# Kernel tuning notes

Measured on AMD Instinct MI355X. Metric: run time of the kernel, lower is better.

## Reference

```python
import jax, jax.numpy as jnp
import numpy as np

HIDDEN = 1024
HEADS = 16
HEAD_D = HIDDEN // HEADS
FILL = -10000.0


def setup_inputs() -> dict:
    key = jax.random.key(0)
    ks = jax.random.split(key, 5)
    scale = 1.0 / np.sqrt(HIDDEN)
    x = jax.random.normal(ks[0], (2, 2048, HIDDEN), dtype=jnp.float32)
    # nn.Linear weights stored as [in, out] (already transposed vs torch)
    W_qkv = jax.random.uniform(ks[1], (HIDDEN, 3 * HIDDEN), dtype=jnp.float32, minval=-scale, maxval=scale)
    b_qkv = jax.random.uniform(ks[2], (3 * HIDDEN,), dtype=jnp.float32, minval=-scale, maxval=scale)
    W_o = jax.random.uniform(ks[3], (HIDDEN, HIDDEN), dtype=jnp.float32, minval=-scale, maxval=scale)
    b_o = jax.random.uniform(ks[4], (HIDDEN,), dtype=jnp.float32, minval=-scale, maxval=scale)
    return {"x": x, "W_qkv": W_qkv, "b_qkv": b_qkv, "W_o": W_o, "b_o": b_o}


def reference(x, W_qkv, b_qkv, W_o, b_o):
    b, s, _ = x.shape
    qkv = x @ W_qkv + b_qkv                       # [b, s, 3*hidden]
    q, k, v = jnp.split(qkv, 3, axis=-1)
    # [b, s, hidden] -> [b, h, s, d]
    def to_heads(t):
        return t.reshape(b, s, HEADS, HEAD_D).transpose(0, 2, 1, 3)
    q, k, v = to_heads(q), to_heads(k), to_heads(v)
    logits = jnp.einsum('bhqd,bhkd->bhqk', q, k) / np.sqrt(HEAD_D).astype(np.float32)
    # Faithful to the original: tril, then fill anything equal to 0 (incl.
    # genuine zeros) with the masked_logit_fill value.
    logits_tril = jnp.tril(logits)
    logits_masked = jnp.where(logits_tril == 0.0, jnp.float32(FILL), logits_tril)
    probs = jax.nn.softmax(logits_masked, axis=-1)
    pre_o = jnp.einsum('bhqk,bhkd->bhqd', probs, v)    # [b, h, s, d]
    pre_o = pre_o.transpose(0, 2, 1, 3).reshape(b, s, HIDDEN)
    return pre_o @ W_o + b_o
```

## Files before the change

### kernel.cpp

```cpp
#include <hip/hip_runtime.h>

typedef __attribute__((ext_vector_type(8))) short short8;
typedef __attribute__((ext_vector_type(4))) short short4b;
typedef __attribute__((ext_vector_type(4))) float f32x4;

static __device__ __forceinline__ short f2bf(float f) {
    unsigned u = __builtin_bit_cast(unsigned, f);
    u += 0x7FFFu + ((u >> 16) & 1u);
    return (short)(u >> 16);
}

static __device__ __forceinline__ void g2l16(const void* g, void* l) {
    __builtin_amdgcn_global_load_lds(
        (const __attribute__((address_space(1))) unsigned*)g,
        (__attribute__((address_space(3))) unsigned*)l, 16, 0, 0);
}

__global__ void convert_x(const float* __restrict__ x, short* __restrict__ xb, int n4) {
    int i = blockIdx.x * blockDim.x + threadIdx.x;
    if (i >= n4) return;
    f32x4 v = *(const f32x4*)&x[(long)i * 4];
    short4b o;
    #pragma unroll
    for (int j = 0; j < 4; ++j) o[j] = f2bf(v[j]);
    *(short4b*)&xb[(long)i * 4] = o;
}

__global__ void transpose_conv(const float* __restrict__ W, short* __restrict__ Wt,
                               int K, int N) {
    __shared__ float lds[64][65];
    const int t = threadIdx.x;
    const int n0 = blockIdx.x * 64, k0 = blockIdx.y * 64;
    const int rr = t >> 4, q4 = (t & 15) * 4;
    #pragma unroll
    for (int p = 0; p < 4; ++p) {
        int k = rr + p * 16;
        f32x4 v = *(const f32x4*)&W[(long)(k0 + k) * N + n0 + q4];
        #pragma unroll
        for (int j = 0; j < 4; ++j) lds[k][q4 + j] = v[j];
    }
    __syncthreads();
    #pragma unroll
    for (int p = 0; p < 4; ++p) {
        int nloc = rr + p * 16;
        short4b o;
        #pragma unroll
        for (int j = 0; j < 4; ++j) o[j] = f2bf(lds[q4 + j][nloc]);
        *(short4b*)&Wt[(long)(n0 + nloc) * K + k0 + q4] = o;
    }
}

template<int F32OUT>
__global__ __launch_bounds__(256, 2)
void gemm_bt(const short* __restrict__ A, const short* __restrict__ Bt,
             const float* __restrict__ bias, void* __restrict__ C,
             int M, int N, int K) {
    __shared__ short lA[128 * 32];
    __shared__ short lB[128 * 32];
    const int t = threadIdx.x;
    const int lane = t & 63, w = t >> 6;
    const int m0 = blockIdx.y * 128, n0 = blockIdx.x * 128;
    const int lr = lane & 15, lk = lane >> 4;
    const int wr = w >> 1, wc = w & 1;

    f32x4 acc[4][4];
    #pragma unroll
    for (int i = 0; i < 4; ++i)
        #pragma unroll
        for (int j = 0; j < 4; ++j)
            #pragma unroll
            for (int e = 0; e < 4; ++e) acc[i][j][e] = 0.0f;

    const int nsteps = K >> 5;
    for (int kt = 0; kt < nsteps; ++kt) {
        const int kb = kt * 32;
        #pragma unroll
        for (int c = 0; c < 2; ++c) {
            int off  = c * 4096 + w * 1024;
            int offl = off + lane * 16;
            int ra = offl >> 6;
            int ca = (offl & 63) >> 1;
            g2l16(A  + (long)(m0 + ra) * K + kb + ca, (short*)lA + (off >> 1));
            g2l16(Bt + (long)(n0 + ra) * K + kb + ca, (short*)lB + (off >> 1));
        }
        __syncthreads();
        short8 af[4], bf[4];
        #pragma unroll
        for (int m = 0; m < 4; ++m)
            af[m] = *(const short8*)&lA[(wr * 64 + m * 16 + lr) * 32 + lk * 8];
        #pragma unroll
        for (int n = 0; n < 4; ++n)
            bf[n] = *(const short8*)&lB[(wc * 64 + n * 16 + lr) * 32 + lk * 8];
        #pragma unroll
        for (int m = 0; m < 4; ++m)
            #pragma unroll
            for (int n = 0; n < 4; ++n)
                acc[m][n] = __builtin_amdgcn_mfma_f32_16x16x32_bf16(af[m], bf[n], acc[m][n], 0, 0, 0);
        __syncthreads();
    }

    #pragma unroll
    for (int n = 0; n < 4; ++n) {
        int col = n0 + wc * 64 + n * 16 + lr;
        float bb = bias[col];
        #pragma unroll
        for (int m = 0; m < 4; ++m) {
            int rowb = m0 + wr * 64 + m * 16 + lk * 4;
            #pragma unroll
            for (int r = 0; r < 4; ++r) {
                float v = acc[m][n][r] + bb;
                if (F32OUT) ((float*)C)[(long)(rowb + r) * N + col] = v;
                else        ((short*)C)[(long)(rowb + r) * N + col] = f2bf(v);
            }
        }
    }
}

__global__ void build_vt(const short* __restrict__ qkv, short* __restrict__ vt) {
    __shared__ short lds[64][72];
    const int t = threadIdx.x;
    const int st = blockIdx.x, bh = blockIdx.y;
    const int b = bh >> 4, h = bh & 15;
    const int s0 = st * 64;
    const int sr = t >> 3, c8 = (t & 7) * 8;
    #pragma unroll
    for (int p = 0; p < 2; ++p) {
        int s = sr + p * 32;
        short8 v = *(const short8*)&qkv[(long)(b * 2048 + s0 + s) * 3072 + 2048 + h * 64 + c8];
        *(short8*)&lds[s][c8] = v;
    }
    __syncthreads();
    #pragma unroll
    for (int p = 0; p < 2; ++p) {
        int d = sr + p * 32;
        short8 v;
        #pragma unroll
        for (int j = 0; j < 8; ++j) v[j] = lds[c8 + j][d];
        *(short8*)&vt[(long)(bh * 64 + d) * 2048 + s0 + c8] = v;
    }
}

__global__ __launch_bounds__(256, 2)
void attn_kernel(const short* __restrict__ qkv, const short* __restrict__ vt,
                 short* __restrict__ pre_o) {
    __shared__ short lK[2][64 * 64];
    __shared__ short lV[2][64 * 64];
    __shared__ short lP[4][16 * 64];
    const int t = threadIdx.x, lane = t & 63, w = t >> 6;
    const int lr = lane & 15, lk = lane >> 4;
    const int pidx = blockIdx.x, bh = blockIdx.y;
    const int b = bh >> 4, h = bh & 15;

    int soff[2], sK_row[2], sslot[2];
    #pragma unroll
    for (int c = 0; c < 2; ++c) {
        int off  = c * 4096 + w * 1024;
        int offl = off + lane * 16;
        int r    = offl >> 7;
        soff[c]  = off >> 1;
        sK_row[c] = r;
        sslot[c] = (((offl >> 4) & 7) ^ (r & 7)) * 8;
    }

    #pragma unroll 1
    for (int seg = 0; seg < 2; ++seg) {
        const int Q  = seg ? (31 - pidx) : pidx;
        const int q0 = Q * 64;
        const int nt = seg ? (32 - pidx) : (pidx + 1);

        short8 aq[2];
        #pragma unroll
        for (int dk = 0; dk < 2; ++dk)
            aq[dk] = *(const short8*)&qkv[(long)(b * 2048 + q0 + w * 16 + lr) * 3072
                                          + h * 64 + dk * 32 + lk * 8];

        f32x4 accO[4];
        #pragma unroll
        for (int n = 0; n < 4; ++n)
            #pragma unroll
            for (int e = 0; e < 4; ++e) accO[n][e] = 0.0f;
        float mst[4], lst[4];
        #pragma unroll
        for (int r = 0; r < 4; ++r) { mst[r] = -1e30f; lst[r] = 0.0f; }

        #pragma unroll
        for (int c = 0; c < 2; ++c) {
            g2l16(qkv + (long)(b * 2048 + 0 * 64 + sK_row[c]) * 3072 + 1024 + h * 64 + sslot[c],
                  &lK[0][soff[c]]);
            g2l16(vt + (long)(bh * 64 + sK_row[c]) * 2048 + 0 * 64 + sslot[c],
                  &lV[0][soff[c]]);
        }
        __syncthreads();

        #pragma unroll 1
        for (int kt = 0; kt < nt; ++kt) {
            const int cur = kt & 1;
            if (kt + 1 < nt) {
                #pragma unroll
                for (int c = 0; c < 2; ++c) {
                    g2l16(qkv + (long)(b * 2048 + (kt + 1) * 64 + sK_row[c]) * 3072
                              + 1024 + h * 64 + sslot[c],
                          &lK[cur ^ 1][soff[c]]);
                    g2l16(vt + (long)(bh * 64 + sK_row[c]) * 2048 + (kt + 1) * 64 + sslot[c],
                          &lV[cur ^ 1][soff[c]]);
                }
            }

            f32x4 accS[4];
            #pragma unroll
            for (int n = 0; n < 4; ++n)
                #pragma unroll
                for (int e = 0; e < 4; ++e) accS[n][e] = 0.0f;
            short8 bk[4][2];
            #pragma unroll
            for (int n = 0; n < 4; ++n)
                #pragma unroll
                for (int dk = 0; dk < 2; ++dk)
                    bk[n][dk] = *(const short8*)((const char*)&lK[cur][0] + (n * 16 + lr) * 128
                                                 + (((dk * 4 + lk) ^ (lr & 7)) << 4));
            #pragma unroll
            for (int n = 0; n < 4; ++n)
                #pragma unroll
                for (int dk = 0; dk < 2; ++dk)
                    accS[n] = __builtin_amdgcn_mfma_f32_16x16x32_bf16(aq[dk], bk[n][dk], accS[n], 0, 0, 0);

            #pragma unroll
            for (int r = 0; r < 4; ++r) {
                int qrow = q0 + w * 16 + lk * 4 + r;
                float sv[4];
                float mx = -1e30f;
                #pragma unroll
                for (int n = 0; n < 4; ++n) {
                    float s = accS[n][r] * 0.125f;
                    int key = kt * 64 + n * 16 + lr;
                    if (key > qrow || s == 0.0f) s = -10000.0f;
                    sv[n] = s;
                    mx = fmaxf(mx, s);
                }
                mx = fmaxf(mx, __shfl_xor(mx, 1));
                mx = fmaxf(mx, __shfl_xor(mx, 2));
                mx = fmaxf(mx, __shfl_xor(mx, 4));
                mx = fmaxf(mx, __shfl_xor(mx, 8));
                float mnew = fmaxf(mst[r], mx);
                float corr = __expf(mst[r] - mnew);
                mst[r] = mnew;
                float rs = 0.0f;
                #pragma unroll
                for (int n = 0; n < 4; ++n) { float p = __expf(sv[n] - mnew); sv[n] = p; rs += p; }
                rs += __shfl_xor(rs, 1);
                rs += __shfl_xor(rs, 2);
                rs += __shfl_xor(rs, 4);
                rs += __shfl_xor(rs, 8);
                lst[r] = lst[r] * corr + rs;
                #pragma unroll
                for (int n = 0; n < 4; ++n) accO[n][r] *= corr;
                int prr = lk * 4 + r;
                int swz = (prr & 7) << 4;
                #pragma unroll
                for (int n = 0; n < 4; ++n) {
                    int pc = n * 16 + lr;
                    *(short*)((char*)&lP[w][0] + prr * 128 + ((pc * 2) ^ swz)) = f2bf(sv[n]);
                }
            }

            short8 ap[2], bv[4][2];
            #pragma unroll
            for (int kk = 0; kk < 2; ++kk)
                ap[kk] = *(const short8*)((const char*)&lP[w][0] + lr * 128
                                          + (((kk * 4 + lk) ^ (lr & 7)) << 4));
            #pragma unroll
            for (int n = 0; n < 4; ++n)
                #pragma unroll
                for (int kk = 0; kk < 2; ++kk)
                    bv[n][kk] = *(const short8*)((const char*)&lV[cur][0] + (n * 16 + lr) * 128
                                                 + (((kk * 4 + lk) ^ (lr & 7)) << 4));
            #pragma unroll
            for (int n = 0; n < 4; ++n)
                #pragma unroll
                for (int kk = 0; kk < 2; ++kk)
                    accO[n] = __builtin_amdgcn_mfma_f32_16x16x32_bf16(ap[kk], bv[n][kk], accO[n], 0, 0, 0);

            __syncthreads();
        }

        #pragma unroll
        for (int r = 0; r < 4; ++r) {
            int qrow = q0 + w * 16 + lk * 4 + r;
            float inv = 1.0f / lst[r];
            #pragma unroll
            for (int n = 0; n < 4; ++n)
                pre_o[(long)(b * 2048 + qrow) * 1024 + h * 64 + n * 16 + lr] =
                    f2bf(accO[n][r] * inv);
        }
    }
}

extern "C" void kernel_launch(void* const* d_in, const int* in_sizes, int n_in,
                              void* d_out, int out_size, void* d_ws, size_t ws_size,
                              hipStream_t stream) {
    const float* x    = (const float*)d_in[0];
    const float* Wqkv = (const float*)d_in[1];
    const float* bqkv = (const float*)d_in[2];
    const float* Wo   = (const float*)d_in[3];
    const float* bo   = (const float*)d_in[4];
    float* out = (float*)d_out;

    char* ws = (char*)d_ws;
    short* xb    = (short*)(ws);
    short* wqkvT = (short*)(ws + (8L  << 20));
    short* woT   = (short*)(ws + (14L << 20));
    short* qkv   = (short*)(ws + (16L << 20));
    short* vt    = (short*)(ws + (40L << 20));
    short* preo  = (short*)(ws + (48L << 20));

    convert_x<<<4096, 256, 0, stream>>>(x, xb, 4096 * 1024 / 4);
    transpose_conv<<<dim3(48, 16), 256, 0, stream>>>(Wqkv, wqkvT, 1024, 3072);
    transpose_conv<<<dim3(16, 16), 256, 0, stream>>>(Wo, woT, 1024, 1024);
    gemm_bt<0><<<dim3(24, 32), 256, 0, stream>>>(xb, wqkvT, bqkv, qkv, 4096, 3072, 1024);
    build_vt<<<dim3(32, 32), 256, 0, stream>>>(qkv, vt);
    attn_kernel<<<dim3(16, 32), 256, 0, stream>>>(qkv, vt, preo);
    gemm_bt<1><<<dim3(8, 32), 256, 0, stream>>>(preo, woT, bo, out, 4096, 1024, 1024);
}
```

Baseline: 224.6 us.

## Use 128-key tiles in attention, fold Q scaling into QKV GEMM, mask only diagonal

The attention inner loop now processes 128 keys per iteration instead of 64, which halves the number of barriers and online-softmax rescale steps and doubles the K/V tiles staged in LDS with wider swizzles. The 1/sqrt(d) scale is moved into the QKV GEMM epilogue for the Q columns, so the attention loop no longer multiplies by it. Causal masking is evaluated only on the final diagonal tile. In exchange, LDS usage and register pressure go up, which may reduce occupancy. The diagonal tile now also computes some fully masked keys. Because Q is rounded to bf16 after scaling by 0.125, the zero-equality fill check could behave slightly differently.

```diff
diff --git a/kernel.cpp b/kernel.cpp
--- a/kernel.cpp
+++ b/kernel.cpp
@@ -50,7 +50,7 @@
     }
 }
 
-template<int F32OUT>
+template<int F32OUT, int QSCALE>
 __global__ __launch_bounds__(256, 2)
 void gemm_bt(const short* __restrict__ A, const short* __restrict__ Bt,
              const float* __restrict__ bias, void* __restrict__ C,
@@ -103,12 +103,13 @@
     for (int n = 0; n < 4; ++n) {
         int col = n0 + wc * 64 + n * 16 + lr;
         float bb = bias[col];
+        float sc = (QSCALE && col < 1024) ? 0.125f : 1.0f;
         #pragma unroll
         for (int m = 0; m < 4; ++m) {
             int rowb = m0 + wr * 64 + m * 16 + lk * 4;
             #pragma unroll
             for (int r = 0; r < 4; ++r) {
-                float v = acc[m][n][r] + bb;
+                float v = (acc[m][n][r] + bb) * sc;
                 if (F32OUT) ((float*)C)[(long)(rowb + r) * N + col] = v;
                 else        ((short*)C)[(long)(rowb + r) * N + col] = f2bf(v);
             }
@@ -143,30 +144,33 @@
 __global__ __launch_bounds__(256, 2)
 void attn_kernel(const short* __restrict__ qkv, const short* __restrict__ vt,
                  short* __restrict__ pre_o) {
-    __shared__ short lK[2][64 * 64];
-    __shared__ short lV[2][64 * 64];
-    __shared__ short lP[4][16 * 64];
+    __shared__ short lK[2][128 * 64];
+    __shared__ short lV[2][64 * 128];
+    __shared__ short lP[4][16 * 128];
     const int t = threadIdx.x, lane = t & 63, w = t >> 6;
     const int lr = lane & 15, lk = lane >> 4;
     const int pidx = blockIdx.x, bh = blockIdx.y;
     const int b = bh >> 4, h = bh & 15;
 
-    int soff[2], sK_row[2], sslot[2];
-    #pragma unroll
-    for (int c = 0; c < 2; ++c) {
+    int soff[4], kRow[4], kCol[4], vRow[4], vCol[4];
+    #pragma unroll
+    for (int c = 0; c < 4; ++c) {
         int off  = c * 4096 + w * 1024;
         int offl = off + lane * 16;
-        int r    = offl >> 7;
-        soff[c]  = off >> 1;
-        sK_row[c] = r;
-        sslot[c] = (((offl >> 4) & 7) ^ (r & 7)) * 8;
+        soff[c] = off >> 1;
+        int kr = offl >> 7;
+        kRow[c] = kr;
+        kCol[c] = ((((offl >> 4) & 7) ^ (kr & 7))) * 8;
+        int vr = offl >> 8;
+        vRow[c] = vr;
+        vCol[c] = ((((offl >> 4) & 15) ^ (vr & 15))) * 8;
     }
 
     #pragma unroll 1
     for (int seg = 0; seg < 2; ++seg) {
         const int Q  = seg ? (31 - pidx) : pidx;
         const int q0 = Q * 64;
-        const int nt = seg ? (32 - pidx) : (pidx + 1);
+        const int nt = (Q >> 1) + 1;
 
         short8 aq[2];
         #pragma unroll
@@ -184,10 +188,10 @@
         for (int r = 0; r < 4; ++r) { mst[r] = -1e30f; lst[r] = 0.0f; }
 
         #pragma unroll
-        for (int c = 0; c < 2; ++c) {
-            g2l16(qkv + (long)(b * 2048 + 0 * 64 + sK_row[c]) * 3072 + 1024 + h * 64 + sslot[c],
+        for (int c = 0; c < 4; ++c) {
+            g2l16(qkv + (long)(b * 2048 + kRow[c]) * 3072 + 1024 + h * 64 + kCol[c],
                   &lK[0][soff[c]]);
-            g2l16(vt + (long)(bh * 64 + sK_row[c]) * 2048 + 0 * 64 + sslot[c],
+            g2l16(vt + (long)(bh * 64 + vRow[c]) * 2048 + vCol[c],
                   &lV[0][soff[c]]);
         }
         __syncthreads();
@@ -197,46 +201,47 @@
             const int cur = kt & 1;
             if (kt + 1 < nt) {
                 #pragma unroll
-                for (int c = 0; c < 2; ++c) {
-                    g2l16(qkv + (long)(b * 2048 + (kt + 1) * 64 + sK_row[c]) * 3072
-                              + 1024 + h * 64 + sslot[c],
+                for (int c = 0; c < 4; ++c) {
+                    g2l16(qkv + (long)(b * 2048 + (kt + 1) * 128 + kRow[c]) * 3072
+                              + 1024 + h * 64 + kCol[c],
                           &lK[cur ^ 1][soff[c]]);
-                    g2l16(vt + (long)(bh * 64 + sK_row[c]) * 2048 + (kt + 1) * 64 + sslot[c],
+                    g2l16(vt + (long)(bh * 64 + vRow[c]) * 2048 + (kt + 1) * 128 + vCol[c],
                           &lV[cur ^ 1][soff[c]]);
                 }
             }
 
-            f32x4 accS[4];
-            #pragma unroll
-            for (int n = 0; n < 4; ++n)
+            f32x4 accS[8];
+            #pragma unroll
+            for (int n = 0; n < 8; ++n) {
                 #pragma unroll
                 for (int e = 0; e < 4; ++e) accS[n][e] = 0.0f;
-            short8 bk[4][2];
-            #pragma unroll
-            for (int n = 0; n < 4; ++n)
-                #pragma unroll
-                for (int dk = 0; dk < 2; ++dk)
-                    bk[n][dk] = *(const short8*)((const char*)&lK[cur][0] + (n * 16 + lr) * 128
-                                                 + (((dk * 4 + lk) ^ (lr & 7)) << 4));
-            #pragma unroll
-            for (int n = 0; n < 4; ++n)
-                #pragma unroll
-                for (int dk = 0; dk < 2; ++dk)
-                    accS[n] = __builtin_amdgcn_mfma_f32_16x16x32_bf16(aq[dk], bk[n][dk], accS[n], 0, 0, 0);
-
+                #pragma unroll
+                for (int dk = 0; dk < 2; ++dk) {
+                    short8 bk = *(const short8*)((const char*)&lK[cur][0]
+                                 + (n * 16 + lr) * 128 + (((dk * 4 + lk) ^ (lr & 7)) << 4));
+                    accS[n] = __builtin_amdgcn_mfma_f32_16x16x32_bf16(aq[dk], bk, accS[n], 0, 0, 0);
+                }
+            }
+
+            const bool diag = (kt == nt - 1);
             #pragma unroll
             for (int r = 0; r < 4; ++r) {
                 int qrow = q0 + w * 16 + lk * 4 + r;
-                float sv[4];
-                float mx = -1e30f;
-                #pragma unroll
-                for (int n = 0; n < 4; ++n) {
-                    float s = accS[n][r] * 0.125f;
-                    int key = kt * 64 + n * 16 + lr;
-                    if (key > qrow || s == 0.0f) s = -10000.0f;
+                float sv[8];
+                #pragma unroll
+                for (int n = 0; n < 8; ++n) {
+                    float s = accS[n][r];
+                    if (diag) {
+                        int key = kt * 128 + n * 16 + lr;
+                        if (key > qrow || s == 0.0f) s = -10000.0f;
+                    } else {
+                        if (s == 0.0f) s = -10000.0f;
+                    }
                     sv[n] = s;
-                    mx = fmaxf(mx, s);
-                }
+                }
+                float mx01 = fmaxf(sv[0], sv[1]), mx23 = fmaxf(sv[2], sv[3]);
+                float mx45 = fmaxf(sv[4], sv[5]), mx67 = fmaxf(sv[6], sv[7]);
+                float mx = fmaxf(fmaxf(mx01, mx23), fmaxf(mx45, mx67));
                 mx = fmaxf(mx, __shfl_xor(mx, 1));
                 mx = fmaxf(mx, __shfl_xor(mx, 2));
                 mx = fmaxf(mx, __shfl_xor(mx, 4));
@@ -246,7 +251,7 @@
                 mst[r] = mnew;
                 float rs = 0.0f;
                 #pragma unroll
-                for (int n = 0; n < 4; ++n) { float p = __expf(sv[n] - mnew); sv[n] = p; rs += p; }
+                for (int n = 0; n < 8; ++n) { float p = __expf(sv[n] - mnew); sv[n] = p; rs += p; }
                 rs += __shfl_xor(rs, 1);
                 rs += __shfl_xor(rs, 2);
                 rs += __shfl_xor(rs, 4);
@@ -255,30 +260,27 @@
                 #pragma unroll
                 for (int n = 0; n < 4; ++n) accO[n][r] *= corr;
                 int prr = lk * 4 + r;
-                int swz = (prr & 7) << 4;
-                #pragma unroll
-                for (int n = 0; n < 4; ++n) {
+                int swz = (prr & 15) << 4;
+                #pragma unroll
+                for (int n = 0; n < 8; ++n) {
                     int pc = n * 16 + lr;
-                    *(short*)((char*)&lP[w][0] + prr * 128 + ((pc * 2) ^ swz)) = f2bf(sv[n]);
+                    *(short*)((char*)&lP[w][0] + prr * 256 + ((pc * 2) ^ swz)) = f2bf(sv[n]);
                 }
             }
 
-            short8 ap[2], bv[4][2];
-            #pragma unroll
-            for (int kk = 0; kk < 2; ++kk)
-                ap[kk] = *(const short8*)((const char*)&lP[w][0] + lr * 128
-                                          + (((kk * 4 + lk) ^ (lr & 7)) << 4));
+            short8 ap[4];
+            #pragma unroll
+            for (int kk = 0; kk < 4; ++kk)
+                ap[kk] = *(const short8*)((const char*)&lP[w][0] + lr * 256
+                                          + (((kk * 4 + lk) ^ (lr & 15)) << 4));
             #pragma unroll
             for (int n = 0; n < 4; ++n)
                 #pragma unroll
-                for (int kk = 0; kk < 2; ++kk)
-                    bv[n][kk] = *(const short8*)((const char*)&lV[cur][0] + (n * 16 + lr) * 128
-                                                 + (((kk * 4 + lk) ^ (lr & 7)) << 4));
-            #pragma unroll
-            for (int n = 0; n < 4; ++n)
-                #pragma unroll
-                for (int kk = 0; kk < 2; ++kk)
-                    accO[n] = __builtin_amdgcn_mfma_f32_16x16x32_bf16(ap[kk], bv[n][kk], accO[n], 0, 0, 0);
+                for (int kk = 0; kk < 4; ++kk) {
+                    short8 bv = *(const short8*)((const char*)&lV[cur][0]
+                                 + (n * 16 + lr) * 256 + (((kk * 4 + lk) ^ (lr & 15)) << 4));
+                    accO[n] = __builtin_amdgcn_mfma_f32_16x16x32_bf16(ap[kk], bv, accO[n], 0, 0, 0);
+                }
 
             __syncthreads();
         }
@@ -316,8 +318,8 @@
     convert_x<<<4096, 256, 0, stream>>>(x, xb, 4096 * 1024 / 4);
     transpose_conv<<<dim3(48, 16), 256, 0, stream>>>(Wqkv, wqkvT, 1024, 3072);
     transpose_conv<<<dim3(16, 16), 256, 0, stream>>>(Wo, woT, 1024, 1024);
-    gemm_bt<0><<<dim3(24, 32), 256, 0, stream>>>(xb, wqkvT, bqkv, qkv, 4096, 3072, 1024);
+    gemm_bt<0, 1><<<dim3(24, 32), 256, 0, stream>>>(xb, wqkvT, bqkv, qkv, 4096, 3072, 1024);
     build_vt<<<dim3(32, 32), 256, 0, stream>>>(qkv, vt);
     attn_kernel<<<dim3(16, 32), 256, 0, stream>>>(qkv, vt, preo);
-    gemm_bt<1><<<dim3(8, 32), 256, 0, stream>>>(preo, woT, bo, out, 4096, 1024, 1024);
-}
+    gemm_bt<1, 0><<<dim3(8, 32), 256, 0, stream>>>(preo, woT, bo, out, 4096, 1024, 1024);
+}
```

Result: no change. 229.0 us (+2.0%).

## Split attention into one block per query tile, fold scale into QKV GEMM

Applied to the files above, without the earlier changes.

The attention kernel no longer pairs a short and a long query tile in one block. It launches one block per 64-row query tile, with the heaviest tiles first, and raises launch bounds to four blocks per CU for more parallelism and occupancy. The 1/8 logit scale now happens in the QKV GEMM epilogue on the Q columns, and the causal index check runs only on the diagonal tile. Scaling Q before rounding to bf16 changes rounding slightly, and the exact-zero test now applies to the scaled product. Per-block prologue overhead doubles because there are twice as many blocks.

```diff
diff --git a/kernel.cpp b/kernel.cpp
--- a/kernel.cpp
+++ b/kernel.cpp
@@ -50,7 +50,7 @@
     }
 }
 
-template<int F32OUT>
+template<int F32OUT, int QSCALE>
 __global__ __launch_bounds__(256, 2)
 void gemm_bt(const short* __restrict__ A, const short* __restrict__ Bt,
              const float* __restrict__ bias, void* __restrict__ C,
@@ -103,12 +103,13 @@
     for (int n = 0; n < 4; ++n) {
         int col = n0 + wc * 64 + n * 16 + lr;
         float bb = bias[col];
+        float sc = (QSCALE && col < 1024) ? 0.125f : 1.0f;
         #pragma unroll
         for (int m = 0; m < 4; ++m) {
             int rowb = m0 + wr * 64 + m * 16 + lk * 4;
             #pragma unroll
             for (int r = 0; r < 4; ++r) {
-                float v = acc[m][n][r] + bb;
+                float v = (acc[m][n][r] + bb) * sc;
                 if (F32OUT) ((float*)C)[(long)(rowb + r) * N + col] = v;
                 else        ((short*)C)[(long)(rowb + r) * N + col] = f2bf(v);
             }
@@ -140,7 +141,7 @@
     }
 }
 
-__global__ __launch_bounds__(256, 2)
+__global__ __launch_bounds__(256, 4)
 void attn_kernel(const short* __restrict__ qkv, const short* __restrict__ vt,
                  short* __restrict__ pre_o) {
     __shared__ short lK[2][64 * 64];
@@ -148,150 +149,142 @@
     __shared__ short lP[4][16 * 64];
     const int t = threadIdx.x, lane = t & 63, w = t >> 6;
     const int lr = lane & 15, lk = lane >> 4;
-    const int pidx = blockIdx.x, bh = blockIdx.y;
+    const int Q = 31 - blockIdx.x;
+    const int bh = blockIdx.y;
     const int b = bh >> 4, h = bh & 15;
-
-    int soff[2], sK_row[2], sslot[2];
+    const int q0 = Q * 64;
+    const int nt = Q + 1;
+
+    int soff[2], sRow[2], sCol[2];
     #pragma unroll
     for (int c = 0; c < 2; ++c) {
         int off  = c * 4096 + w * 1024;
         int offl = off + lane * 16;
         int r    = offl >> 7;
         soff[c]  = off >> 1;
-        sK_row[c] = r;
-        sslot[c] = (((offl >> 4) & 7) ^ (r & 7)) * 8;
-    }
+        sRow[c]  = r;
+        sCol[c]  = (((offl >> 4) & 7) ^ (r & 7)) * 8;
+    }
+
+    short8 aq[2];
+    #pragma unroll
+    for (int dk = 0; dk < 2; ++dk)
+        aq[dk] = *(const short8*)&qkv[(long)(b * 2048 + q0 + w * 16 + lr) * 3072
+                                      + h * 64 + dk * 32 + lk * 8];
+
+    f32x4 accO[4];
+    #pragma unroll
+    for (int n = 0; n < 4; ++n)
+        #pragma unroll
+        for (int e = 0; e < 4; ++e) accO[n][e] = 0.0f;
+    float mst[4], lst[4];
+    #pragma unroll
+    for (int r = 0; r < 4; ++r) { mst[r] = -1e30f; lst[r] = 0.0f; }
+
+    #pragma unroll
+    for (int c = 0; c < 2; ++c) {
+        g2l16(qkv + (long)(b * 2048 + sRow[c]) * 3072 + 1024 + h * 64 + sCol[c],
+              &lK[0][soff[c]]);
+        g2l16(vt + (long)(bh * 64 + sRow[c]) * 2048 + sCol[c],
+              &lV[0][soff[c]]);
+    }
+    __syncthreads();
 
     #pragma unroll 1
-    for (int seg = 0; seg < 2; ++seg) {
-        const int Q  = seg ? (31 - pidx) : pidx;
-        const int q0 = Q * 64;
-        const int nt = seg ? (32 - pidx) : (pidx + 1);
-
-        short8 aq[2];
-        #pragma unroll
-        for (int dk = 0; dk < 2; ++dk)
-            aq[dk] = *(const short8*)&qkv[(long)(b * 2048 + q0 + w * 16 + lr) * 3072
-                                          + h * 64 + dk * 32 + lk * 8];
-
-        f32x4 accO[4];
-        #pragma unroll
-        for (int n = 0; n < 4; ++n)
-            #pragma unroll
-            for (int e = 0; e < 4; ++e) accO[n][e] = 0.0f;
-        float mst[4], lst[4];
-        #pragma unroll
-        for (int r = 0; r < 4; ++r) { mst[r] = -1e30f; lst[r] = 0.0f; }
-
-        #pragma unroll
-        for (int c = 0; c < 2; ++c) {
-            g2l16(qkv + (long)(b * 2048 + 0 * 64 + sK_row[c]) * 3072 + 1024 + h * 64 + sslot[c],
-                  &lK[0][soff[c]]);
-            g2l16(vt + (long)(bh * 64 + sK_row[c]) * 2048 + 0 * 64 + sslot[c],
-                  &lV[0][soff[c]]);
-        }
-        __syncthreads();
-
-        #pragma unroll 1
-        for (int kt = 0; kt < nt; ++kt) {
-            const int cur = kt & 1;
-            if (kt + 1 < nt) {
-                #pragma unroll
-                for (int c = 0; c < 2; ++c) {
-                    g2l16(qkv + (long)(b * 2048 + (kt + 1) * 64 + sK_row[c]) * 3072
-                              + 1024 + h * 64 + sslot[c],
-                          &lK[cur ^ 1][soff[c]]);
-                    g2l16(vt + (long)(bh * 64 + sK_row[c]) * 2048 + (kt + 1) * 64 + sslot[c],
-                          &lV[cur ^ 1][soff[c]]);
-                }
-            }
-
-            f32x4 accS[4];
-            #pragma unroll
-            for (int n = 0; n < 4; ++n)
-                #pragma unroll
-                for (int e = 0; e < 4; ++e) accS[n][e] = 0.0f;
-            short8 bk[4][2];
-            #pragma unroll
-            for (int n = 0; n < 4; ++n)
-                #pragma unroll
-                for (int dk = 0; dk < 2; ++dk)
-                    bk[n][dk] = *(const short8*)((const char*)&lK[cur][0] + (n * 16 + lr) * 128
-                                                 + (((dk * 4 + lk) ^ (lr & 7)) << 4));
-            #pragma unroll
-            for (int n = 0; n < 4; ++n)
-                #pragma unroll
-                for (int dk = 0; dk < 2; ++dk)
-                    accS[n] = __builtin_amdgcn_mfma_f32_16x16x32_bf16(aq[dk], bk[n][dk], accS[n], 0, 0, 0);
-
-            #pragma unroll
-            for (int r = 0; r < 4; ++r) {
-                int qrow = q0 + w * 16 + lk * 4 + r;
-                float sv[4];
-                float mx = -1e30f;
-                #pragma unroll
-                for (int n = 0; n < 4; ++n) {
-                    float s = accS[n][r] * 0.125f;
+    for (int kt = 0; kt < nt; ++kt) {
+        const int cur = kt & 1;
+        if (kt + 1 < nt) {
+            #pragma unroll
+            for (int c = 0; c < 2; ++c) {
+                g2l16(qkv + (long)(b * 2048 + (kt + 1) * 64 + sRow[c]) * 3072
+                          + 1024 + h * 64 + sCol[c],
+                      &lK[cur ^ 1][soff[c]]);
+                g2l16(vt + (long)(bh * 64 + sRow[c]) * 2048 + (kt + 1) * 64 + sCol[c],
+                      &lV[cur ^ 1][soff[c]]);
+            }
+        }
+
+        f32x4 accS[4];
+        #pragma unroll
+        for (int n = 0; n < 4; ++n) {
+            #pragma unroll
+            for (int e = 0; e < 4; ++e) accS[n][e] = 0.0f;
+            #pragma unroll
+            for (int dk = 0; dk < 2; ++dk) {
+                short8 bk = *(const short8*)((const char*)&lK[cur][0]
+                             + (n * 16 + lr) * 128 + (((dk * 4 + lk) ^ (lr & 7)) << 4));
+                accS[n] = __builtin_amdgcn_mfma_f32_16x16x32_bf16(aq[dk], bk, accS[n], 0, 0, 0);
+            }
+        }
+
+        const bool diag = (kt == nt - 1);
+        #pragma unroll
+        for (int r = 0; r < 4; ++r) {
+            int qrow = q0 + w * 16 + lk * 4 + r;
+            float sv[4];
+            #pragma unroll
+            for (int n = 0; n < 4; ++n) {
+                float s = accS[n][r];
+                if (diag) {
                     int key = kt * 64 + n * 16 + lr;
                     if (key > qrow || s == 0.0f) s = -10000.0f;
-                    sv[n] = s;
-                    mx = fmaxf(mx, s);
+                } else {
+                    if (s == 0.0f) s = -10000.0f;
                 }
-                mx = fmaxf(mx, __shfl_xor(mx, 1));
-                mx = fmaxf(mx, __shfl_xor(mx, 2));
-                mx = fmaxf(mx, __shfl_xor(mx, 4));
-                mx = fmaxf(mx, __shfl_xor(mx, 8));
-                float mnew = fmaxf(mst[r], mx);
-                float corr = __expf(mst[r] - mnew);
-                mst[r] = mnew;
-                float rs = 0.0f;
-                #pragma unroll
-                for (int n = 0; n < 4; ++n) { float p = __expf(sv[n] - mnew); sv[n] = p; rs += p; }
-                rs += __shfl_xor(rs, 1);
-                rs += __shfl_xor(rs, 2);
-                rs += __shfl_xor(rs, 4);
-                rs += __shfl_xor(rs, 8);
-                lst[r] = lst[r] * corr + rs;
-                #pragma unroll
-                for (int n = 0; n < 4; ++n) accO[n][r] *= corr;
-                int prr = lk * 4 + r;
-                int swz = (prr & 7) << 4;
-                #pragma unroll
-                for (int n = 0; n < 4; ++n) {
-                    int pc = n * 16 + lr;
-                    *(short*)((char*)&lP[w][0] + prr * 128 + ((pc * 2) ^ swz)) = f2bf(sv[n]);
-                }
-            }
-
-            short8 ap[2], bv[4][2];
-            #pragma unroll
-            for (int kk = 0; kk < 2; ++kk)
-                ap[kk] = *(const short8*)((const char*)&lP[w][0] + lr * 128
-                                          + (((kk * 4 + lk) ^ (lr & 7)) << 4));
-            #pragma unroll
-            for (int n = 0; n < 4; ++n)
-                #pragma unroll
-                for (int kk = 0; kk < 2; ++kk)
-                    bv[n][kk] = *(const short8*)((const char*)&lV[cur][0] + (n * 16 + lr) * 128
-                                                 + (((kk * 4 + lk) ^ (lr & 7)) << 4));
-            #pragma unroll
-            for (int n = 0; n < 4; ++n)
-                #pragma unroll
-                for (int kk = 0; kk < 2; ++kk)
-                    accO[n] = __builtin_amdgcn_mfma_f32_16x16x32_bf16(ap[kk], bv[n][kk], accO[n], 0, 0, 0);
-
-            __syncthreads();
-        }
-
-        #pragma unroll
-        for (int r = 0; r < 4; ++r) {
-            int qrow = q0 + w * 16 + lk * 4 + r;
-            float inv = 1.0f / lst[r];
-            #pragma unroll
-            for (int n = 0; n < 4; ++n)
-                pre_o[(long)(b * 2048 + qrow) * 1024 + h * 64 + n * 16 + lr] =
-                    f2bf(accO[n][r] * inv);
-        }
+                sv[n] = s;
+            }
+            float mx = fmaxf(fmaxf(sv[0], sv[1]), fmaxf(sv[2], sv[3]));
+            mx = fmaxf(mx, __shfl_xor(mx, 1));
+            mx = fmaxf(mx, __shfl_xor(mx, 2));
+            mx = fmaxf(mx, __shfl_xor(mx, 4));
+            mx = fmaxf(mx, __shfl_xor(mx, 8));
+            float mnew = fmaxf(mst[r], mx);
+            float corr = __expf(mst[r] - mnew);
+            mst[r] = mnew;
+            float rs = 0.0f;
+            #pragma unroll
+            for (int n = 0; n < 4; ++n) { float p = __expf(sv[n] - mnew); sv[n] = p; rs += p; }
+            rs += __shfl_xor(rs, 1);
+            rs += __shfl_xor(rs, 2);
+            rs += __shfl_xor(rs, 4);
+            rs += __shfl_xor(rs, 8);
+            lst[r] = lst[r] * corr + rs;
+            #pragma unroll
+            for (int n = 0; n < 4; ++n) accO[n][r] *= corr;
+            int prr = lk * 4 + r;
+            int swz = (prr & 7) << 4;
+            #pragma unroll
+            for (int n = 0; n < 4; ++n) {
+                int pc = n * 16 + lr;
+                *(short*)((char*)&lP[w][0] + prr * 128 + ((pc * 2) ^ swz)) = f2bf(sv[n]);
+            }
+        }
+
+        short8 ap[2];
+        #pragma unroll
+        for (int kk = 0; kk < 2; ++kk)
+            ap[kk] = *(const short8*)((const char*)&lP[w][0] + lr * 128
+                                      + (((kk * 4 + lk) ^ (lr & 7)) << 4));
+        #pragma unroll
+        for (int n = 0; n < 4; ++n)
+            #pragma unroll
+            for (int kk = 0; kk < 2; ++kk) {
+                short8 bv = *(const short8*)((const char*)&lV[cur][0]
+                             + (n * 16 + lr) * 128 + (((kk * 4 + lk) ^ (lr & 7)) << 4));
+                accO[n] = __builtin_amdgcn_mfma_f32_16x16x32_bf16(ap[kk], bv, accO[n], 0, 0, 0);
+            }
+
+        __syncthreads();
+    }
+
+    #pragma unroll
+    for (int r = 0; r < 4; ++r) {
+        int qrow = q0 + w * 16 + lk * 4 + r;
+        float inv = 1.0f / lst[r];
+        #pragma unroll
+        for (int n = 0; n < 4; ++n)
+            pre_o[(long)(b * 2048 + qrow) * 1024 + h * 64 + n * 16 + lr] =
+                f2bf(accO[n][r] * inv);
     }
 }
 
@@ -316,8 +309,8 @@
     convert_x<<<4096, 256, 0, stream>>>(x, xb, 4096 * 1024 / 4);
     transpose_conv<<<dim3(48, 16), 256, 0, stream>>>(Wqkv, wqkvT, 1024, 3072);
     transpose_conv<<<dim3(16, 16), 256, 0, stream>>>(Wo, woT, 1024, 1024);
-    gemm_bt<0><<<dim3(24, 32), 256, 0, stream>>>(xb, wqkvT, bqkv, qkv, 4096, 3072, 1024);
+    gemm_bt<0, 1><<<dim3(24, 32), 256, 0, stream>>>(xb, wqkvT, bqkv, qkv, 4096, 3072, 1024);
     build_vt<<<dim3(32, 32), 256, 0, stream>>>(qkv, vt);
-    attn_kernel<<<dim3(16, 32), 256, 0, stream>>>(qkv, vt, preo);
-    gemm_bt<1><<<dim3(8, 32), 256, 0, stream>>>(preo, woT, bo, out, 4096, 1024, 1024);
-}
+    attn_kernel<<<dim3(32, 32), 256, 0, stream>>>(qkv, vt, preo);
+    gemm_bt<1, 0><<<dim3(8, 32), 256, 0, stream>>>(preo, woT, bo, out, 4096, 1024, 1024);
+}
```

Result: slower. 260.8 us (+16.2%).
